# Performance work log

Hardware: AMD Instinct MI355X
Metric: run time of the kernel (lower is better)

## Reference

```python
import jax, jax.numpy as jnp
import numpy as np

D = 256                      # covariance dim, hardcoded by bottleneck Conv2d(_, 256, 1)
ITER_N = 5                   # SqrtmLayer(output, 5)
_r, _c = np.triu_indices(D)
FLAT_IDX = jnp.asarray(_r * D + _c)   # upper-tri (incl. diag) indices into flattened d*d


def setup_inputs() -> dict:
    key = jax.random.key(0)
    ks = jax.random.split(key, 5)
    B, C, H, W = 64, 2048, 16, 16
    num_classes = 4
    feats = D * (D + 1) // 2  # 32896
    return {
        "features": jax.random.normal(ks[0], (B, C, H, W), jnp.float32),
        "w_bn": jax.random.normal(ks[1], (D, C), jnp.float32) * 0.02,
        "b_bn": jnp.zeros((D,), jnp.float32),
        "w_type": jax.random.normal(ks[2], (num_classes, feats), jnp.float32) * 0.01,
        "b_type": jnp.zeros((num_classes,), jnp.float32),
        "w_flag": jax.random.normal(ks[3], (1, feats), jnp.float32) * 0.01,
        "b_flag": jnp.zeros((1,), jnp.float32),
    }


def _covpool(x):
    # x: [B, d, h, w] -> second-order pooling: x_f @ I_hat @ x_f^T, equivalent
    # to (1/M) * centered @ centered^T  (I_hat = -1/M^2 * ones + 1/M * eye)
    B, d, h, w = x.shape
    M = h * w
    xf = x.reshape(B, d, M)
    centered = xf - xf.mean(axis=2, keepdims=True)
    return jnp.einsum('bim,bjm->bij', centered, centered) / M  # [B, d, d]


def _sqrtm_ns(A, iter_n=ITER_N):
    # Newton-Schulz iteration for matrix square root (iSQRT-COV style)
    B, d, _ = A.shape
    I3 = 3.0 * jnp.eye(d, dtype=A.dtype)
    normA = jnp.trace(A, axis1=1, axis2=2)          # [B], pre-normalization
    An = A / normA[:, None, None]
    ZY = 0.5 * (I3 - An)
    Y = jnp.matmul(An, ZY)
    Z = ZY
    for _ in range(iter_n - 2):
        ZY = 0.5 * (I3 - jnp.matmul(Z, Y))
        Y = jnp.matmul(Y, ZY)
        Z = jnp.matmul(ZY, Z)
    YZY = 0.5 * jnp.matmul(Y, I3 - jnp.matmul(Z, Y))
    return YZY * jnp.sqrt(normA)[:, None, None]     # post-compensation


def reference(features, w_bn, b_bn, w_type, b_type, w_flag, b_flag):
    # 1x1 bottleneck conv: [B, C, H, W] -> [B, 256, H, W]
    x = jnp.einsum('bchw,oc->bohw', features, w_bn) + b_bn[None, :, None, None]
    cov = _covpool(x)                # [B, 256, 256]
    s = _sqrtm_ns(cov)               # [B, 256, 256]
    B = s.shape[0]
    vec = s.reshape(B, D * D)[:, FLAT_IDX]   # triu-vec: [B, 32896]
    type_logits = vec @ w_type.T + b_type    # [B, num_classes]
    flag_logits = vec @ w_flag.T + b_flag    # [B, 1]
    return (type_logits, flag_logits)
```

## Files before the change

### kernel.cpp

```cpp
#include <hip/hip_runtime.h>
#include <math.h>


typedef __attribute__((ext_vector_type(8))) short bf16x8;
typedef __attribute__((ext_vector_type(4))) float f32x4;
typedef __attribute__((ext_vector_type(4))) unsigned u32x4;
typedef __attribute__((ext_vector_type(2))) unsigned u32x2;

__device__ __forceinline__ unsigned fbits(float f) { union { float f; unsigned u; } x; x.f = f; return x.u; }
__device__ __forceinline__ float bitsf(unsigned u) { union { float f; unsigned u; } x; x.u = u; return x.f; }
__device__ __forceinline__ float bf16v(short h) { return bitsf(((unsigned)(unsigned short)h) << 16); }

__device__ __forceinline__ unsigned pack_h(float a, float b) {
  return (fbits(a) >> 16) | (fbits(b) & 0xFFFF0000u);
}
__device__ __forceinline__ unsigned pack_l(float a, float b) {
  float la = a - bitsf(fbits(a) & 0xFFFF0000u);
  float lb = b - bitsf(fbits(b) & 0xFFFF0000u);
  return (fbits(la) >> 16) | (fbits(lb) & 0xFFFF0000u);
}

__device__ __forceinline__ const bf16x8* fragp(const char* M, int kt, int row,
                                               int g, int pl) {
  return (const bf16x8*)(M + (size_t)kt * 32768 + (size_t)row * 128 +
                         ((((pl << 2) + g) ^ (row & 7)) << 4));
}
__device__ __forceinline__ const bf16x8* fragl(const char* L, int kt, int row,
                                               int g, int pl) {
  return (const bf16x8*)(L + kt * 8192 + row * 128 +
                         ((((pl << 2) + g) ^ (row & 7)) << 4));
}

__device__ __forceinline__ void write_quad_g(char* M, int row, int k0,
                                             const float* v) {
  char* rp = M + (size_t)(k0 >> 5) * 32768 + (size_t)row * 128;
  const int s = (k0 & 31) >> 3, bo = (k0 & 7) * 2;
  *(u32x2*)(rp + (((s) ^ (row & 7)) << 4) + bo) =
      (u32x2){pack_h(v[0], v[1]), pack_h(v[2], v[3])};
  *(u32x2*)(rp + (((s + 4) ^ (row & 7)) << 4) + bo) =
      (u32x2){pack_l(v[0], v[1]), pack_l(v[2], v[3])};
}
__device__ __forceinline__ void write_quad_l(char* L, int row, int k0,
                                             const float* v) {
  char* rp = L + (k0 >> 5) * 8192 + row * 128;
  const int s = (k0 & 31) >> 3, bo = (k0 & 7) * 2;
  *(u32x2*)(rp + (((s) ^ (row & 7)) << 4) + bo) =
      (u32x2){pack_h(v[0], v[1]), pack_h(v[2], v[3])};
  *(u32x2*)(rp + (((s + 4) ^ (row & 7)) << 4) + bo) =
      (u32x2){pack_l(v[0], v[1]), pack_l(v[2], v[3])};
}
__device__ __forceinline__ void read_quad_g(const char* M, int row, int k0,
                                            float* v) {
  const char* rp = M + (size_t)(k0 >> 5) * 32768 + (size_t)row * 128;
  const int s = (k0 & 31) >> 3, bo = (k0 & 7) * 2;
  const u32x2 hq = *(const u32x2*)(rp + (((s) ^ (row & 7)) << 4) + bo);
  const u32x2 lq = *(const u32x2*)(rp + (((s + 4) ^ (row & 7)) << 4) + bo);
  v[0] = bitsf(hq[0] << 16) + bitsf(lq[0] << 16);
  v[1] = bitsf(hq[0] & 0xFFFF0000u) + bitsf(lq[0] & 0xFFFF0000u);
  v[2] = bitsf(hq[1] << 16) + bitsf(lq[1] << 16);
  v[3] = bitsf(hq[1] & 0xFFFF0000u) + bitsf(lq[1] & 0xFFFF0000u);
}

#define MFMA3(c, aH, aL, bH, bL)                                            \
  c = __builtin_amdgcn_mfma_f32_16x16x32_bf16(aL, bH, c, 0, 0, 0);          \
  c = __builtin_amdgcn_mfma_f32_16x16x32_bf16(aH, bL, c, 0, 0, 0);          \
  c = __builtin_amdgcn_mfma_f32_16x16x32_bf16(aH, bH, c, 0, 0, 0);

__global__ __launch_bounds__(256) void conv_k(
    const char* __restrict__ Wf, const float* __restrict__ F,
    char* __restrict__ X, const float* __restrict__ bias)
{
  const int tid = threadIdx.x, lane = tid & 63, w = tid >> 6;
  const int wr = w >> 1, wc = w & 1, fr = lane & 15, g = lane >> 4;
  const int bz = blockIdx.z, ib = blockIdx.y * 128, jb = blockIdx.x * 64;
  const float* Fb = F + (size_t)bz * 524288;

  f32x4 acc[4][2] = {};
  bf16x8 pa[2][4][2];
  float xv[2][16];

#pragma unroll
  for (int par = 0; par < 2; ++par) {
#pragma unroll
    for (int m = 0; m < 4; ++m) {
      const int r = ib + wr * 64 + m * 16 + fr;
#pragma unroll
      for (int pl = 0; pl < 2; ++pl) pa[par][m][pl] = *fragp(Wf, par, r, g, pl);
    }
    const float* src = Fb + ((size_t)par * 32 + g * 8) * 256 + jb + wc * 32 + fr;
#pragma unroll
    for (int n = 0; n < 2; ++n)
#pragma unroll
      for (int e = 0; e < 8; ++e) xv[par][n * 8 + e] = src[e * 256 + n * 16];
  }

  for (int t2 = 0; t2 < 64; t2 += 2) {
#pragma unroll
    for (int par = 0; par < 2; ++par) {
      const int t = t2 + par;
      bf16x8 aH[4], aL[4];
#pragma unroll
      for (int m = 0; m < 4; ++m) { aH[m] = pa[par][m][0]; aL[m] = pa[par][m][1]; }
      bf16x8 bH[2], bL[2];
#pragma unroll
      for (int n = 0; n < 2; ++n) {
        short hh[8], ll[8];
#pragma unroll
        for (int e = 0; e < 8; ++e) {
          const float v = xv[par][n * 8 + e];
          const unsigned u = fbits(v);
          hh[e] = (short)(u >> 16);
          ll[e] = (short)(fbits(v - bitsf(u & 0xFFFF0000u)) >> 16);
        }
        bH[n] = *(bf16x8*)hh; bL[n] = *(bf16x8*)ll;
      }
      if (t + 2 < 64) {
#pragma unroll
        for (int m = 0; m < 4; ++m) {
          const int r = ib + wr * 64 + m * 16 + fr;
#pragma unroll
          for (int pl = 0; pl < 2; ++pl)
            pa[par][m][pl] = *fragp(Wf, t + 2, r, g, pl);
        }
        const float* src =
            Fb + ((size_t)(t + 2) * 32 + g * 8) * 256 + jb + wc * 32 + fr;
#pragma unroll
        for (int n = 0; n < 2; ++n)
#pragma unroll
          for (int e = 0; e < 8; ++e)
            xv[par][n * 8 + e] = src[e * 256 + n * 16];
      }
#pragma unroll
      for (int m = 0; m < 4; ++m)
#pragma unroll
        for (int n = 0; n < 2; ++n) {
          f32x4 c = acc[m][n];
          MFMA3(c, aH[m], aL[m], bH[n], bL[n]);
          acc[m][n] = c;
        }
    }
  }

  char* Xb = X + (size_t)bz * 262144;
#pragma unroll
  for (int m = 0; m < 4; ++m) {
    const int gi0 = ib + wr * 64 + m * 16 + g * 4;
#pragma unroll
    for (int n = 0; n < 2; ++n) {
      const int gj = jb + wc * 32 + n * 16 + fr;
      const int ktj = gj >> 5, sj = (gj & 31) >> 3, bo = (gj & 7) * 2;
#pragma unroll
      for (int j = 0; j < 4; ++j) {
        const int gi = gi0 + j;
        char* rp = Xb + (size_t)ktj * 32768 + (size_t)gi * 128;
        const float v = acc[m][n][j] + bias[gi];
        const unsigned u = fbits(v);
        *(short*)(rp + ((sj ^ (gi & 7)) << 4) + bo) = (short)(u >> 16);
        *(short*)(rp + (((sj + 4) ^ (gi & 7)) << 4) + bo) =
            (short)(fbits(v - bitsf(u & 0xFFFF0000u)) >> 16);
      }
    }
  }
}

template <int MODE>
__global__ __launch_bounds__(512) void col_k(
    const char* __restrict__ A1, const char* __restrict__ Bsrc,
    const char* __restrict__ Ys, const char* __restrict__ Zs,
    char* __restrict__ outA, char* __restrict__ outB,
    const float* __restrict__ mu, const float* __restrict__ nrm,
    float* __restrict__ Sf)
{
  __shared__ __align__(16) char Plds[65536];
  const int tid = threadIdx.x, lane = tid & 63, w = tid >> 6;
  const int fr = lane & 15, g = lane >> 4;
  const int blk = blockIdx.x;
  const int bz = (blk & 7) * 8 + ((blk >> 3) & 7);
  const int jb = (blk >> 6) * 64;
  const size_t MB = 262144;
  const char* Ab = A1 + (size_t)bz * MB;
  const char* Bb = Bsrc + (size_t)bz * MB;
  const int r0 = g * 4;

  f32x4 acc[2][4] = {};
  {
    bf16x8 pa[2][2][2], pb[2][4][2];
#pragma unroll
    for (int par = 0; par < 2; ++par) {
#pragma unroll
      for (int m = 0; m < 2; ++m) {
        const int r = w * 32 + m * 16 + fr;
#pragma unroll
        for (int pl = 0; pl < 2; ++pl) pa[par][m][pl] = *fragp(Ab, par, r, g, pl);
      }
#pragma unroll
      for (int n = 0; n < 4; ++n) {
        const int r = jb + n * 16 + fr;
#pragma unroll
        for (int pl = 0; pl < 2; ++pl) pb[par][n][pl] = *fragp(Bb, par, r, g, pl);
      }
    }
    for (int t2 = 0; t2 < 8; t2 += 2) {
#pragma unroll
      for (int par = 0; par < 2; ++par) {
        const int t = t2 + par;
        bf16x8 aH[2], aL[2], bH[4], bL[4];
#pragma unroll
        for (int m = 0; m < 2; ++m) { aH[m] = pa[par][m][0]; aL[m] = pa[par][m][1]; }
#pragma unroll
        for (int n = 0; n < 4; ++n) { bH[n] = pb[par][n][0]; bL[n] = pb[par][n][1]; }
        if (t + 2 < 8) {
#pragma unroll
          for (int m = 0; m < 2; ++m) {
            const int r = w * 32 + m * 16 + fr;
#pragma unroll
            for (int pl = 0; pl < 2; ++pl)
              pa[par][m][pl] = *fragp(Ab, t + 2, r, g, pl);
          }
#pragma unroll
          for (int n = 0; n < 4; ++n) {
            const int r = jb + n * 16 + fr;
#pragma unroll
            for (int pl = 0; pl < 2; ++pl)
              pb[par][n][pl] = *fragp(Bb, t + 2, r, g, pl);
          }
        }
#pragma unroll
        for (int m = 0; m < 2; ++m)
#pragma unroll
          for (int n = 0; n < 4; ++n) {
            f32x4 c = acc[m][n];
            MFMA3(c, aH[m], aL[m], bH[n], bL[n]);
            acc[m][n] = c;
          }
      }
    }
  }

  if constexpr (MODE == 0) {
    const float rn = 1.0f / nrm[bz];
    const float* mub = mu + bz * 256;
    char* oA = outA + (size_t)bz * MB;
    char* oB = outB + (size_t)bz * MB;
#pragma unroll
    for (int m = 0; m < 2; ++m) {
      const int gi0 = w * 32 + m * 16 + r0;
#pragma unroll
      for (int n = 0; n < 4; ++n) {
        const int gj = jb + n * 16 + fr;
        float vv[4], zz[4];
#pragma unroll
        for (int j = 0; j < 4; ++j) {
          const float v =
              (acc[m][n][j] * (1.f / 256.f) - mub[gi0 + j] * mub[gj]) * rn;
          vv[j] = v;
          zz[j] = (gi0 + j == gj ? 1.5f : 0.f) - 0.5f * v;
        }
        write_quad_g(oA, gj, gi0, vv);
        write_quad_g(oB, gj, gi0, zz);
      }
    }
  } else if constexpr (MODE == 1) {
    char* oA = outA + (size_t)bz * MB;
#pragma unroll
    for (int m = 0; m < 2; ++m) {
      const int gi0 = w * 32 + m * 16 + r0;
#pragma unroll
      for (int n = 0; n < 4; ++n) {
        const int gj = jb + n * 16 + fr;
        float av[4], vv[4];
        read_quad_g(Bb, gj, gi0, av);
#pragma unroll
        for (int j = 0; j < 4; ++j) vv[j] = 1.5f * av[j] - 0.5f * acc[m][n][j];
        write_quad_g(oA, gj, gi0, vv);
      }
    }
  } else {
#pragma unroll
    for (int m = 0; m < 2; ++m) {
      const int gi0 = w * 32 + m * 16 + r0;
#pragma unroll
      for (int n = 0; n < 4; ++n) {
        const int jl = n * 16 + fr;
        float vv[4] = {acc[m][n][0], acc[m][n][1], acc[m][n][2], acc[m][n][3]};
        write_quad_l(Plds, jl, gi0, vv);
      }
    }
    __syncthreads();

    const char* Yb = Ys + (size_t)bz * MB;
    const char* Zb = (MODE == 2) ? (Zs + (size_t)bz * MB) : nullptr;
    f32x4 aY[2][4] = {}, aZ[2][4] = {};
    bf16x8 py[2][2][2], pz[2][2][2];
#pragma unroll
    for (int par = 0; par < 2; ++par)
#pragma unroll
      for (int m = 0; m < 2; ++m) {
        const int r = w * 32 + m * 16 + fr;
#pragma unroll
        for (int pl = 0; pl < 2; ++pl) {
          py[par][m][pl] = *fragp(Yb, par, r, g, pl);
          if constexpr (MODE == 2) pz[par][m][pl] = *fragp(Zb, par, r, g, pl);
        }
      }
    for (int t2 = 0; t2 < 8; t2 += 2) {
#pragma unroll
      for (int par = 0; par < 2; ++par) {
        const int t = t2 + par;
        bf16x8 yH[2], yL[2], zH[2], zL[2];
#pragma unroll
        for (int m = 0; m < 2; ++m) {
          yH[m] = py[par][m][0]; yL[m] = py[par][m][1];
          if constexpr (MODE == 2) { zH[m] = pz[par][m][0]; zL[m] = pz[par][m][1]; }
        }
        if (t + 2 < 8) {
#pragma unroll
          for (int m = 0; m < 2; ++m) {
            const int r = w * 32 + m * 16 + fr;
#pragma unroll
            for (int pl = 0; pl < 2; ++pl) {
              py[par][m][pl] = *fragp(Yb, t + 2, r, g, pl);
              if constexpr (MODE == 2) pz[par][m][pl] = *fragp(Zb, t + 2, r, g, pl);
            }
          }
        }
        bf16x8 bH[4], bL[4];
#pragma unroll
        for (int n = 0; n < 4; ++n) {
          const int jl = n * 16 + fr;
          bH[n] = *fragl(Plds, t, jl, g, 0);
          bL[n] = *fragl(Plds, t, jl, g, 1);
        }
#pragma unroll
        for (int m = 0; m < 2; ++m)
#pragma unroll
          for (int n = 0; n < 4; ++n) {
            f32x4 cy = aY[m][n];
            MFMA3(cy, yH[m], yL[m], bH[n], bL[n]);
            aY[m][n] = cy;
            if constexpr (MODE == 2) {
              f32x4 cz = aZ[m][n];
              MFMA3(cz, zH[m], zL[m], bH[n], bL[n]);
              aZ[m][n] = cz;
            }
          }
      }
    }
    if constexpr (MODE == 2) {
      char* oA = outA + (size_t)bz * MB;
      char* oB = outB + (size_t)bz * MB;
#pragma unroll
      for (int m = 0; m < 2; ++m) {
        const int gi0 = w * 32 + m * 16 + r0;
#pragma unroll
        for (int n = 0; n < 4; ++n) {
          const int gj = jb + n * 16 + fr;
          float base[4], vv[4];
          read_quad_g(Yb, gj, gi0, base);
#pragma unroll
          for (int j = 0; j < 4; ++j) vv[j] = 1.5f * base[j] - 0.5f * aY[m][n][j];
          write_quad_g(oA, gj, gi0, vv);
          read_quad_g(Zb, gj, gi0, base);
#pragma unroll
          for (int j = 0; j < 4; ++j) vv[j] = 1.5f * base[j] - 0.5f * aZ[m][n][j];
          write_quad_g(oB, gj, gi0, vv);
        }
      }
    } else {
      const float sq = sqrtf(nrm[bz]);
      float* Sb = Sf + (size_t)bz * 65536;
#pragma unroll
      for (int m = 0; m < 2; ++m) {
        const int gi0 = w * 32 + m * 16 + r0;
#pragma unroll
        for (int n = 0; n < 4; ++n) {
          const int gj = jb + n * 16 + fr;
          float base[4];
          read_quad_g(Yb, gj, gi0, base);
          f32x4 vv;
#pragma unroll
          for (int j = 0; j < 4; ++j)
            vv[j] = (1.5f * base[j] - 0.5f * aY[m][n][j]) * sq;
          *(f32x4*)(Sb + (size_t)gj * 256 + gi0) = vv;
        }
      }
    }
  }
}

__global__ __launch_bounds__(256) void cvt_w(const float* __restrict__ wsrc,
                                             char* __restrict__ Wf)
{
  const int kt = blockIdx.x, r = threadIdx.x;
  const float* src = wsrc + (size_t)r * 2048 + kt * 32;
  char* rp = Wf + (size_t)kt * 32768 + (size_t)r * 128;
#pragma unroll
  for (int s = 0; s < 4; ++s) {
    float x[8];
#pragma unroll
    for (int e = 0; e < 8; ++e) x[e] = src[s * 8 + e];
    *(u32x4*)(rp + ((s ^ (r & 7)) << 4)) =
        (u32x4){pack_h(x[0], x[1]), pack_h(x[2], x[3]), pack_h(x[4], x[5]), pack_h(x[6], x[7])};
    *(u32x4*)(rp + (((s + 4) ^ (r & 7)) << 4)) =
        (u32x4){pack_l(x[0], x[1]), pack_l(x[2], x[3]), pack_l(x[4], x[5]), pack_l(x[6], x[7])};
  }
}

__global__ __launch_bounds__(256) void build_w2(const float* __restrict__ w_type,
                                                const float* __restrict__ w_flag,
                                                float* __restrict__ W2)
{
  const int v = blockIdx.x >> 6, chunk = blockIdx.x & 63;
  const float* src = (v < 4) ? (w_type + (size_t)v * 32896) : w_flag;
  const int e0 = chunk * 1024 + threadIdx.x * 4;
#pragma unroll
  for (int q = 0; q < 4; ++q) {
    const int e = e0 + q;
    const int i = e >> 8, j = e & 255;
    const int r = i < j ? i : j, c = i < j ? j : i;
    const int t = r * 256 - (r * (r - 1)) / 2 + (c - r);
    W2[(size_t)v * 65536 + e] = src[t] * (i == j ? 1.0f : 0.5f);
  }
}

__global__ __launch_bounds__(256) void meanvar(const char* __restrict__ X,
                                               float* __restrict__ mu,
                                               float* __restrict__ nrm)
{
  const int b = blockIdx.x, i = threadIdx.x;
  const char* rp0 = X + (size_t)b * 262144 + (size_t)i * 128;
  float s = 0.f, ss = 0.f;
  for (int kt = 0; kt < 8; ++kt) {
    const char* rp = rp0 + kt * 32768;
#pragma unroll
    for (int sl = 0; sl < 4; ++sl) {
      bf16x8 h8 = *(const bf16x8*)(rp + ((sl ^ (i & 7)) << 4));
      bf16x8 l8 = *(const bf16x8*)(rp + (((sl + 4) ^ (i & 7)) << 4));
#pragma unroll
      for (int e = 0; e < 8; ++e) {
        const float v = bf16v(h8[e]) + bf16v(l8[e]);
        s += v; ss += v * v;
      }
    }
  }
  const float m = s * (1.f / 256.f);
  mu[b * 256 + i] = m;
  __shared__ float red[256];
  red[i] = ss * (1.f / 256.f) - m * m;
  __syncthreads();
  for (int o = 128; o > 0; o >>= 1) {
    if (i < o) red[i] += red[i + o];
    __syncthreads();
  }
  if (i == 0) nrm[b] = red[0];
}

__global__ __launch_bounds__(256) void head2(
    const float* __restrict__ Sf, const float* __restrict__ W2,
    const float* __restrict__ b_type, const float* __restrict__ b_flag,
    float* __restrict__ out)
{
  const int b = blockIdx.x, v = blockIdx.y, tid = threadIdx.x;
  const float4* s4 = (const float4*)(Sf + (size_t)b * 65536);
  const float4* w4 = (const float4*)(W2 + (size_t)v * 65536);
  float acc = 0.f;
  for (int i = tid; i < 16384; i += 256) {
    const float4 a = s4[i], c = w4[i];
    acc += a.x * c.x + a.y * c.y + a.z * c.z + a.w * c.w;
  }
  __shared__ float red[256];
  red[tid] = acc;
  __syncthreads();
  for (int o = 128; o > 0; o >>= 1) {
    if (tid < o) red[tid] += red[tid + o];
    __syncthreads();
  }
  if (tid == 0) {
    if (v < 4) out[b * 4 + v] = red[0] + b_type[v];
    else       out[256 + b] = red[0] + b_flag[0];
  }
}

extern "C" void kernel_launch(void* const* d_in, const int* in_sizes, int n_in,
                              void* d_out, int out_size, void* d_ws, size_t ws_size,
                              hipStream_t stream)
{
  const float* features = (const float*)d_in[0];
  const float* w_bn     = (const float*)d_in[1];
  const float* b_bn     = (const float*)d_in[2];
  const float* w_type   = (const float*)d_in[3];
  const float* b_type   = (const float*)d_in[4];
  const float* w_flag   = (const float*)d_in[5];
  const float* b_flag   = (const float*)d_in[6];
  float* out = (float*)d_out;

  char* W = (char*)d_ws;
  const size_t PB = 16777216;
  char* P0 = W;           char* P1 = W + PB;     char* P2 = W + 2 * PB;
  char* P3 = W + 3 * PB;  char* P4 = W + 4 * PB;
  char* Wf = W + 5 * PB;
  float* W2 = (float*)Wf;
  float* mu = (float*)(W + 5 * PB + 2097152);
  float* nrm = mu + 64 * 256;
  float* Sf = (float*)P4;

  cvt_w<<<dim3(64), dim3(256), 0, stream>>>(w_bn, Wf);
  conv_k<<<dim3(4, 2, 64), dim3(256), 0, stream>>>(Wf, features, P0, b_bn);
  build_w2<<<dim3(320), dim3(256), 0, stream>>>(w_type, w_flag, W2);
  meanvar<<<dim3(64), dim3(256), 0, stream>>>(P0, mu, nrm);

  const dim3 cg(256), cb(512);
  col_k<0><<<cg, cb, 0, stream>>>(P0, P0, nullptr, nullptr, P1, P2, mu, nrm, nullptr);
  col_k<1><<<cg, cb, 0, stream>>>(P1, P1, nullptr, nullptr, P3, nullptr, nullptr, nullptr, nullptr);
  col_k<2><<<cg, cb, 0, stream>>>(P2, P3, P3, P2, P0, P4, nullptr, nullptr, nullptr);
  col_k<2><<<cg, cb, 0, stream>>>(P4, P0, P0, P4, P1, P2, nullptr, nullptr, nullptr);
  col_k<2><<<cg, cb, 0, stream>>>(P2, P1, P1, P2, P3, P0, nullptr, nullptr, nullptr);
  col_k<3><<<cg, cb, 0, stream>>>(P0, P3, P3, nullptr, nullptr, nullptr, nullptr, nrm, Sf);

  head2<<<dim3(64, 5), dim3(256), 0, stream>>>(Sf, W2, b_type, b_flag, out);
  (void)in_sizes; (void)n_in; (void)out_size; (void)ws_size;
}
```

Baseline: 280.2 us.

## Pre-transpose features to split-bf16 swizzled layout before bottleneck conv GEMM

Adds a transpose kernel that converts the fp32 features into a pre-split hi/lo bf16, swizzled, K-tiled layout, processed in two halves of 32 batches that reuse the P1 scratch buffer. The conv GEMM then loads both operands as MFMA fragments directly, with no per-iteration fp32-to-bf16 splitting and no strided scalar loads. Output tiles shrink to 64x64, giving more blocks. The cost is an extra pass over the 128MB feature tensor (read fp32, write the same size of split bf16, read it again) plus two additional launches.

```diff
diff --git a/kernel.cpp b/kernel.cpp
--- a/kernel.cpp
+++ b/kernel.cpp
@@ -66,72 +66,83 @@
   c = __builtin_amdgcn_mfma_f32_16x16x32_bf16(aH, bL, c, 0, 0, 0);          \
   c = __builtin_amdgcn_mfma_f32_16x16x32_bf16(aH, bH, c, 0, 0, 0);
 
-__global__ __launch_bounds__(256) void conv_k(
-    const char* __restrict__ Wf, const float* __restrict__ F,
-    char* __restrict__ X, const float* __restrict__ bias)
+__global__ __launch_bounds__(256) void transp_k(const float* __restrict__ F,
+                                                char* __restrict__ Ft, int b0)
+{
+  const int kt = blockIdx.x, bl = blockIdx.y, px = threadIdx.x;
+  const float* src = F + ((size_t)(b0 + bl) * 2048 + (size_t)kt * 32) * 256 + px;
+  float v[32];
+#pragma unroll
+  for (int c = 0; c < 32; ++c) v[c] = src[(size_t)c * 256];
+  char* rp = Ft + (size_t)bl * 2097152 + (size_t)kt * 32768 + (size_t)px * 128;
+#pragma unroll
+  for (int s = 0; s < 4; ++s) {
+    const float* x = v + s * 8;
+    *(u32x4*)(rp + ((s ^ (px & 7)) << 4)) =
+        (u32x4){pack_h(x[0], x[1]), pack_h(x[2], x[3]),
+                pack_h(x[4], x[5]), pack_h(x[6], x[7])};
+    *(u32x4*)(rp + (((s + 4) ^ (px & 7)) << 4)) =
+        (u32x4){pack_l(x[0], x[1]), pack_l(x[2], x[3]),
+                pack_l(x[4], x[5]), pack_l(x[6], x[7])};
+  }
+}
+
+__global__ __launch_bounds__(256) void conv2_k(
+    const char* __restrict__ Wf, const char* __restrict__ Ft,
+    char* __restrict__ X, const float* __restrict__ bias, int b0)
 {
   const int tid = threadIdx.x, lane = tid & 63, w = tid >> 6;
   const int wr = w >> 1, wc = w & 1, fr = lane & 15, g = lane >> 4;
-  const int bz = blockIdx.z, ib = blockIdx.y * 128, jb = blockIdx.x * 64;
-  const float* Fb = F + (size_t)bz * 524288;
-
-  f32x4 acc[4][2] = {};
-  bf16x8 pa[2][4][2];
-  float xv[2][16];
+  const int bz = b0 + blockIdx.z;
+  const char* Fb = Ft + (size_t)blockIdx.z * 2097152;
+  const int ib = blockIdx.y * 64, jb = blockIdx.x * 64;
+
+  f32x4 acc[2][2] = {};
+  bf16x8 pa[2][2][2], pb[2][2][2];
 
 #pragma unroll
   for (int par = 0; par < 2; ++par) {
 #pragma unroll
-    for (int m = 0; m < 4; ++m) {
-      const int r = ib + wr * 64 + m * 16 + fr;
+    for (int m = 0; m < 2; ++m) {
+      const int r = ib + wr * 32 + m * 16 + fr;
 #pragma unroll
       for (int pl = 0; pl < 2; ++pl) pa[par][m][pl] = *fragp(Wf, par, r, g, pl);
     }
-    const float* src = Fb + ((size_t)par * 32 + g * 8) * 256 + jb + wc * 32 + fr;
-#pragma unroll
-    for (int n = 0; n < 2; ++n)
-#pragma unroll
-      for (int e = 0; e < 8; ++e) xv[par][n * 8 + e] = src[e * 256 + n * 16];
+#pragma unroll
+    for (int n = 0; n < 2; ++n) {
+      const int r = jb + wc * 32 + n * 16 + fr;
+#pragma unroll
+      for (int pl = 0; pl < 2; ++pl) pb[par][n][pl] = *fragp(Fb, par, r, g, pl);
+    }
   }
 
   for (int t2 = 0; t2 < 64; t2 += 2) {
 #pragma unroll
     for (int par = 0; par < 2; ++par) {
       const int t = t2 + par;
-      bf16x8 aH[4], aL[4];
-#pragma unroll
-      for (int m = 0; m < 4; ++m) { aH[m] = pa[par][m][0]; aL[m] = pa[par][m][1]; }
-      bf16x8 bH[2], bL[2];
-#pragma unroll
-      for (int n = 0; n < 2; ++n) {
-        short hh[8], ll[8];
-#pragma unroll
-        for (int e = 0; e < 8; ++e) {
-          const float v = xv[par][n * 8 + e];
-          const unsigned u = fbits(v);
-          hh[e] = (short)(u >> 16);
-          ll[e] = (short)(fbits(v - bitsf(u & 0xFFFF0000u)) >> 16);
-        }
-        bH[n] = *(bf16x8*)hh; bL[n] = *(bf16x8*)ll;
-      }
+      bf16x8 aH[2], aL[2], bH[2], bL[2];
+#pragma unroll
+      for (int m = 0; m < 2; ++m) { aH[m] = pa[par][m][0]; aL[m] = pa[par][m][1]; }
+#pragma unroll
+      for (int n = 0; n < 2; ++n) { bH[n] = pb[par][n][0]; bL[n] = pb[par][n][1]; }
       if (t + 2 < 64) {
 #pragma unroll
-        for (int m = 0; m < 4; ++m) {
-          const int r = ib + wr * 64 + m * 16 + fr;
+        for (int m = 0; m < 2; ++m) {
+          const int r = ib + wr * 32 + m * 16 + fr;
 #pragma unroll
           for (int pl = 0; pl < 2; ++pl)
             pa[par][m][pl] = *fragp(Wf, t + 2, r, g, pl);
         }
-        const float* src =
-            Fb + ((size_t)(t + 2) * 32 + g * 8) * 256 + jb + wc * 32 + fr;
-#pragma unroll
-        for (int n = 0; n < 2; ++n)
-#pragma unroll
-          for (int e = 0; e < 8; ++e)
-            xv[par][n * 8 + e] = src[e * 256 + n * 16];
-      }
-#pragma unroll
-      for (int m = 0; m < 4; ++m)
+#pragma unroll
+        for (int n = 0; n < 2; ++n) {
+          const int r = jb + wc * 32 + n * 16 + fr;
+#pragma unroll
+          for (int pl = 0; pl < 2; ++pl)
+            pb[par][n][pl] = *fragp(Fb, t + 2, r, g, pl);
+        }
+      }
+#pragma unroll
+      for (int m = 0; m < 2; ++m)
 #pragma unroll
         for (int n = 0; n < 2; ++n) {
           f32x4 c = acc[m][n];
@@ -143,8 +154,8 @@
 
   char* Xb = X + (size_t)bz * 262144;
 #pragma unroll
-  for (int m = 0; m < 4; ++m) {
-    const int gi0 = ib + wr * 64 + m * 16 + g * 4;
+  for (int m = 0; m < 2; ++m) {
+    const int gi0 = ib + wr * 32 + m * 16 + g * 4;
 #pragma unroll
     for (int n = 0; n < 2; ++n) {
       const int gj = jb + wc * 32 + n * 16 + fr;
@@ -503,9 +514,14 @@
   float* mu = (float*)(W + 5 * PB + 2097152);
   float* nrm = mu + 64 * 256;
   float* Sf = (float*)P4;
+  char* Ft = P1;
 
   cvt_w<<<dim3(64), dim3(256), 0, stream>>>(w_bn, Wf);
-  conv_k<<<dim3(4, 2, 64), dim3(256), 0, stream>>>(Wf, features, P0, b_bn);
+  transp_k<<<dim3(64, 32), dim3(256), 0, stream>>>(features, Ft, 0);
+  conv2_k<<<dim3(4, 4, 32), dim3(256), 0, stream>>>(Wf, Ft, P0, b_bn, 0);
+  transp_k<<<dim3(64, 32), dim3(256), 0, stream>>>(features, Ft, 32);
+  conv2_k<<<dim3(4, 4, 32), dim3(256), 0, stream>>>(Wf, Ft, P0, b_bn, 32);
+
   build_w2<<<dim3(320), dim3(256), 0, stream>>>(w_type, w_flag, W2);
   meanvar<<<dim3(64), dim3(256), 0, stream>>>(P0, mu, nrm);
 
```

After: 355.9 us. +27.0%, slower.

## Pre-split features to bf16 hi/lo layout and stage conv tiles via LDS

Applied to the files above, without the earlier changes.

Adds a prep kernel that converts the input features into a swizzled bf16 hi/lo tiled layout and also absorbs the weight conversion and head-weight build into one launch. The conv kernel now streams A and B tiles into a triple-buffered LDS ring with async global-to-LDS loads, instead of per-lane strided fp32 loads and in-register splitting. A sync point in the column kernel is moved after the prefetch loads. The cost is an extra full write and read of the features (about 128 MB of intermediate in workspace) in exchange for coalesced pipelined loads in the GEMM.

```diff
diff --git a/kernel.cpp b/kernel.cpp
--- a/kernel.cpp
+++ b/kernel.cpp
@@ -61,84 +61,130 @@
   v[3] = bitsf(hq[1] & 0xFFFF0000u) + bitsf(lq[1] & 0xFFFF0000u);
 }
 
+__device__ __forceinline__ void gld16(const void* g, void* l) {
+  __builtin_amdgcn_global_load_lds(
+      (const __attribute__((address_space(1))) void*)(size_t)(g),
+      (__attribute__((address_space(3))) void*)(unsigned)(size_t)(l), 16, 0, 0);
+}
+
+#define WAIT_VM(N) asm volatile("s_waitcnt vmcnt(" #N ")" ::: "memory")
+#define BARRIER() do { __builtin_amdgcn_s_barrier(); asm volatile("" ::: "memory"); } while (0)
+
 #define MFMA3(c, aH, aL, bH, bL)                                            \
   c = __builtin_amdgcn_mfma_f32_16x16x32_bf16(aL, bH, c, 0, 0, 0);          \
   c = __builtin_amdgcn_mfma_f32_16x16x32_bf16(aH, bL, c, 0, 0, 0);          \
   c = __builtin_amdgcn_mfma_f32_16x16x32_bf16(aH, bH, c, 0, 0, 0);
 
-__global__ __launch_bounds__(256) void conv_k(
-    const char* __restrict__ Wf, const float* __restrict__ F,
+__global__ __launch_bounds__(256) void prep_k(
+    const float* __restrict__ F, const float* __restrict__ w_bn,
+    const float* __restrict__ w_type, const float* __restrict__ w_flag,
+    char* __restrict__ Ft, char* __restrict__ Wf, float* __restrict__ W2)
+{
+  const int bid = blockIdx.x;
+  if (bid < 4096) {
+    const int kt = bid & 63, bl = bid >> 6, px = threadIdx.x;
+    const float* src = F + ((size_t)bl * 2048 + (size_t)kt * 32) * 256 + px;
+    float v[32];
+#pragma unroll
+    for (int c = 0; c < 32; ++c) v[c] = src[(size_t)c * 256];
+    char* rp = Ft + (size_t)bl * 2097152 + (size_t)kt * 32768 + (size_t)px * 128;
+#pragma unroll
+    for (int s = 0; s < 4; ++s) {
+      const float* x = v + s * 8;
+      *(u32x4*)(rp + ((s ^ (px & 7)) << 4)) =
+          (u32x4){pack_h(x[0], x[1]), pack_h(x[2], x[3]),
+                  pack_h(x[4], x[5]), pack_h(x[6], x[7])};
+      *(u32x4*)(rp + (((s + 4) ^ (px & 7)) << 4)) =
+          (u32x4){pack_l(x[0], x[1]), pack_l(x[2], x[3]),
+                  pack_l(x[4], x[5]), pack_l(x[6], x[7])};
+    }
+  } else if (bid < 4160) {
+    const int kt = bid - 4096, r = threadIdx.x;
+    const float* src = w_bn + (size_t)r * 2048 + kt * 32;
+    char* rp = Wf + (size_t)kt * 32768 + (size_t)r * 128;
+#pragma unroll
+    for (int s = 0; s < 4; ++s) {
+      float x[8];
+#pragma unroll
+      for (int e = 0; e < 8; ++e) x[e] = src[s * 8 + e];
+      *(u32x4*)(rp + ((s ^ (r & 7)) << 4)) =
+          (u32x4){pack_h(x[0], x[1]), pack_h(x[2], x[3]),
+                  pack_h(x[4], x[5]), pack_h(x[6], x[7])};
+      *(u32x4*)(rp + (((s + 4) ^ (r & 7)) << 4)) =
+          (u32x4){pack_l(x[0], x[1]), pack_l(x[2], x[3]),
+                  pack_l(x[4], x[5]), pack_l(x[6], x[7])};
+    }
+  } else {
+    const int idx = bid - 4160;
+    const int v = idx >> 6, chunk = idx & 63;
+    const float* src = (v < 4) ? (w_type + (size_t)v * 32896) : w_flag;
+    const int e0 = chunk * 1024 + threadIdx.x * 4;
+#pragma unroll
+    for (int q = 0; q < 4; ++q) {
+      const int e = e0 + q;
+      const int i = e >> 8, j = e & 255;
+      const int r = i < j ? i : j, c = i < j ? j : i;
+      const int t = r * 256 - (r * (r - 1)) / 2 + (c - r);
+      W2[(size_t)v * 65536 + e] = src[t] * (i == j ? 1.0f : 0.5f);
+    }
+  }
+}
+
+__global__ __launch_bounds__(256) void conv3_k(
+    const char* __restrict__ Wf, const char* __restrict__ Ft,
     char* __restrict__ X, const float* __restrict__ bias)
 {
+  __shared__ __align__(16) char lds[3 * 24576];
   const int tid = threadIdx.x, lane = tid & 63, w = tid >> 6;
   const int wr = w >> 1, wc = w & 1, fr = lane & 15, g = lane >> 4;
   const int bz = blockIdx.z, ib = blockIdx.y * 128, jb = blockIdx.x * 64;
-  const float* Fb = F + (size_t)bz * 524288;
+  const char* Fb = Ft + (size_t)bz * 2097152;
 
   f32x4 acc[4][2] = {};
-  bf16x8 pa[2][4][2];
-  float xv[2][16];
-
-#pragma unroll
-  for (int par = 0; par < 2; ++par) {
+
+  auto stage = [&](int t) {
+    char* L = lds + (t % 3) * 24576;
+    const char* Ag = Wf + (size_t)t * 32768 + (size_t)ib * 128;
+    const char* Bg = Fb + (size_t)t * 32768 + (size_t)jb * 128;
+#pragma unroll
+    for (int i = 0; i < 6; ++i) {
+      const int c = w + i * 4;
+      if (c < 16) gld16(Ag + c * 1024 + lane * 16, L + c * 1024);
+      else        gld16(Bg + (c - 16) * 1024 + lane * 16, L + 16384 + (c - 16) * 1024);
+    }
+  };
+
+  stage(0); stage(1);
+  for (int t = 0; t < 64; ++t) {
+    if (t < 62)      { WAIT_VM(12); }
+    else if (t == 62){ WAIT_VM(6); }
+    else             { WAIT_VM(0); }
+    BARRIER();
+    if (t + 2 < 64) stage(t + 2);
+    const char* L = lds + (t % 3) * 24576;
+    bf16x8 aH[4], aL[4], bH[2], bL[2];
 #pragma unroll
     for (int m = 0; m < 4; ++m) {
-      const int r = ib + wr * 64 + m * 16 + fr;
-#pragma unroll
-      for (int pl = 0; pl < 2; ++pl) pa[par][m][pl] = *fragp(Wf, par, r, g, pl);
-    }
-    const float* src = Fb + ((size_t)par * 32 + g * 8) * 256 + jb + wc * 32 + fr;
-#pragma unroll
-    for (int n = 0; n < 2; ++n)
-#pragma unroll
-      for (int e = 0; e < 8; ++e) xv[par][n * 8 + e] = src[e * 256 + n * 16];
-  }
-
-  for (int t2 = 0; t2 < 64; t2 += 2) {
-#pragma unroll
-    for (int par = 0; par < 2; ++par) {
-      const int t = t2 + par;
-      bf16x8 aH[4], aL[4];
-#pragma unroll
-      for (int m = 0; m < 4; ++m) { aH[m] = pa[par][m][0]; aL[m] = pa[par][m][1]; }
-      bf16x8 bH[2], bL[2];
+      const int r = wr * 64 + m * 16 + fr;
+      const char* p = L + r * 128;
+      aH[m] = *(const bf16x8*)(p + ((g ^ (r & 7)) << 4));
+      aL[m] = *(const bf16x8*)(p + (((g + 4) ^ (r & 7)) << 4));
+    }
+#pragma unroll
+    for (int n = 0; n < 2; ++n) {
+      const int r = wc * 32 + n * 16 + fr;
+      const char* p = L + 16384 + r * 128;
+      bH[n] = *(const bf16x8*)(p + ((g ^ (r & 7)) << 4));
+      bL[n] = *(const bf16x8*)(p + (((g + 4) ^ (r & 7)) << 4));
+    }
+#pragma unroll
+    for (int m = 0; m < 4; ++m)
 #pragma unroll
       for (int n = 0; n < 2; ++n) {
-        short hh[8], ll[8];
-#pragma unroll
-        for (int e = 0; e < 8; ++e) {
-          const float v = xv[par][n * 8 + e];
-          const unsigned u = fbits(v);
-          hh[e] = (short)(u >> 16);
-          ll[e] = (short)(fbits(v - bitsf(u & 0xFFFF0000u)) >> 16);
-        }
-        bH[n] = *(bf16x8*)hh; bL[n] = *(bf16x8*)ll;
-      }
-      if (t + 2 < 64) {
-#pragma unroll
-        for (int m = 0; m < 4; ++m) {
-          const int r = ib + wr * 64 + m * 16 + fr;
-#pragma unroll
-          for (int pl = 0; pl < 2; ++pl)
-            pa[par][m][pl] = *fragp(Wf, t + 2, r, g, pl);
-        }
-        const float* src =
-            Fb + ((size_t)(t + 2) * 32 + g * 8) * 256 + jb + wc * 32 + fr;
-#pragma unroll
-        for (int n = 0; n < 2; ++n)
-#pragma unroll
-          for (int e = 0; e < 8; ++e)
-            xv[par][n * 8 + e] = src[e * 256 + n * 16];
-      }
-#pragma unroll
-      for (int m = 0; m < 4; ++m)
-#pragma unroll
-        for (int n = 0; n < 2; ++n) {
-          f32x4 c = acc[m][n];
-          MFMA3(c, aH[m], aL[m], bH[n], bL[n]);
-          acc[m][n] = c;
-        }
-    }
+        f32x4 c = acc[m][n];
+        MFMA3(c, aH[m], aL[m], bH[n], bL[n]);
+        acc[m][n] = c;
+      }
   }
 
   char* Xb = X + (size_t)bz * 262144;
@@ -286,11 +332,8 @@
         write_quad_l(Plds, jl, gi0, vv);
       }
     }
-    __syncthreads();
-
     const char* Yb = Ys + (size_t)bz * MB;
     const char* Zb = (MODE == 2) ? (Zs + (size_t)bz * MB) : nullptr;
-    f32x4 aY[2][4] = {}, aZ[2][4] = {};
     bf16x8 py[2][2][2], pz[2][2][2];
 #pragma unroll
     for (int par = 0; par < 2; ++par)
@@ -303,6 +346,9 @@
           if constexpr (MODE == 2) pz[par][m][pl] = *fragp(Zb, par, r, g, pl);
         }
       }
+    __syncthreads();
+
+    f32x4 aY[2][4] = {}, aZ[2][4] = {};
     for (int t2 = 0; t2 < 8; t2 += 2) {
 #pragma unroll
       for (int par = 0; par < 2; ++par) {
@@ -385,41 +431,6 @@
         }
       }
     }
-  }
-}
-
-__global__ __launch_bounds__(256) void cvt_w(const float* __restrict__ wsrc,
-                                             char* __restrict__ Wf)
-{
-  const int kt = blockIdx.x, r = threadIdx.x;
-  const float* src = wsrc + (size_t)r * 2048 + kt * 32;
-  char* rp = Wf + (size_t)kt * 32768 + (size_t)r * 128;
-#pragma unroll
-  for (int s = 0; s < 4; ++s) {
-    float x[8];
-#pragma unroll
-    for (int e = 0; e < 8; ++e) x[e] = src[s * 8 + e];
-    *(u32x4*)(rp + ((s ^ (r & 7)) << 4)) =
-        (u32x4){pack_h(x[0], x[1]), pack_h(x[2], x[3]), pack_h(x[4], x[5]), pack_h(x[6], x[7])};
-    *(u32x4*)(rp + (((s + 4) ^ (r & 7)) << 4)) =
-        (u32x4){pack_l(x[0], x[1]), pack_l(x[2], x[3]), pack_l(x[4], x[5]), pack_l(x[6], x[7])};
-  }
-}
-
-__global__ __launch_bounds__(256) void build_w2(const float* __restrict__ w_type,
-                                                const float* __restrict__ w_flag,
-                                                float* __restrict__ W2)
-{
-  const int v = blockIdx.x >> 6, chunk = blockIdx.x & 63;
-  const float* src = (v < 4) ? (w_type + (size_t)v * 32896) : w_flag;
-  const int e0 = chunk * 1024 + threadIdx.x * 4;
-#pragma unroll
-  for (int q = 0; q < 4; ++q) {
-    const int e = e0 + q;
-    const int i = e >> 8, j = e & 255;
-    const int r = i < j ? i : j, c = i < j ? j : i;
-    const int t = r * 256 - (r * (r - 1)) / 2 + (c - r);
-    W2[(size_t)v * 65536 + e] = src[t] * (i == j ? 1.0f : 0.5f);
   }
 }
 
@@ -499,14 +510,15 @@
   char* P0 = W;           char* P1 = W + PB;     char* P2 = W + 2 * PB;
   char* P3 = W + 3 * PB;  char* P4 = W + 4 * PB;
   char* Wf = W + 5 * PB;
-  float* W2 = (float*)Wf;
   float* mu = (float*)(W + 5 * PB + 2097152);
   float* nrm = mu + 64 * 256;
+  char* Ft = W + 5 * PB + 4194304;
+  float* W2 = (float*)(Ft + 64ull * 2097152);
   float* Sf = (float*)P4;
 
-  cvt_w<<<dim3(64), dim3(256), 0, stream>>>(w_bn, Wf);
-  conv_k<<<dim3(4, 2, 64), dim3(256), 0, stream>>>(Wf, features, P0, b_bn);
-  build_w2<<<dim3(320), dim3(256), 0, stream>>>(w_type, w_flag, W2);
+  prep_k<<<dim3(4480), dim3(256), 0, stream>>>(features, w_bn, w_type, w_flag,
+                                               Ft, Wf, W2);
+  conv3_k<<<dim3(4, 2, 64), dim3(256), 0, stream>>>(Wf, Ft, P0, b_bn);
   meanvar<<<dim3(64), dim3(256), 0, stream>>>(P0, mu, nrm);
 
   const dim3 cg(256), cb(512);
```

After: 344.7 us. +23.0%, slower.
